# Optimization experiments

Hardware: AMD Instinct MI355X
Metric: run time of the kernel (lower is better)

The kernel has to match this reference:

```python
import jax, jax.numpy as jnp
import numpy as np

N = 100000   # nodes
E = 1600000  # edges
IN = 128     # in_feats
H = 3        # num_heads
D = 16       # out_feats per head
K = 3        # hops
NEG_SLOPE = 0.2
EPS = 1e-9


def leaky(x):
    return jnp.where(x >= 0, x, NEG_SLOPE * x)


def segment_softmax(e, idx, n):
    # e: [E, H] scores, softmax over edges sharing the same idx (node)
    m = jax.ops.segment_max(e, idx, num_segments=n)
    ex = jnp.exp(e - m[idx])
    s = jax.ops.segment_sum(ex, idx, num_segments=n)
    return ex / s[idx]


def feat_trans(h, i, norm_scales, offsets, pos_emb):
    # per-hop mean/var normalization (biased var) + position embedding
    mean = h.mean(axis=-1, keepdims=True)
    var = h.var(axis=-1, keepdims=True) + EPS
    h = (h - mean) * norm_scales[i] * jax.lax.rsqrt(var) + offsets[i]
    return h + pos_emb[:, :, i, :]


def setup_inputs() -> dict:
    key = jax.random.key(0)
    ks = jax.random.split(key, 10)
    s = 0.1
    feat = jax.random.normal(ks[0], (N, IN), jnp.float32)
    src = jax.random.randint(ks[1], (E,), 0, N)
    dst = jax.random.randint(ks[2], (E,), 0, N)
    fc_W = jax.random.normal(ks[3], (IN, H * D), jnp.float32) * s
    attn_l = jax.random.normal(ks[4], (1, H, D), jnp.float32) * s
    attn_r = jax.random.normal(ks[5], (1, H, D), jnp.float32) * s
    hop_attn_l = jax.random.normal(ks[6], (1, H, D), jnp.float32) * s
    hop_attn_r = jax.random.normal(ks[7], (1, H, D), jnp.float32) * s
    pos_emb = jax.random.normal(ks[8], (1, H, K + 1, D), jnp.float32) * s
    norm_scales = jnp.ones((K + 1, 1, H, D), jnp.float32)
    offsets = jnp.zeros((K + 1, 1, H, D), jnp.float32)
    bias = jnp.zeros((H * D,), jnp.float32)
    return dict(feat=feat, src=src, dst=dst, fc_W=fc_W, attn_l=attn_l,
                attn_r=attn_r, hop_attn_l=hop_attn_l, hop_attn_r=hop_attn_r,
                pos_emb=pos_emb, norm_scales=norm_scales, offsets=offsets,
                bias=bias)


def reference(feat, src, dst, fc_W, attn_l, attn_r, hop_attn_l, hop_attn_r,
              pos_emb, norm_scales, offsets, bias):
    ft = (feat @ fc_W).reshape(N, H, D)            # [N,H,D]
    el = (ft * attn_l).sum(-1)                      # [N,H]
    er = (ft * attn_r).sum(-1)                      # [N,H]
    e = leaky(el[src] + er[dst])                    # [E,H]
    a_dst = jnp.clip(segment_softmax(e, dst, N), EPS, None)
    a_src = jnp.clip(segment_softmax(e, src, N), EPS, None)
    a = jnp.sqrt(a_dst * a_src)                     # [E,H] symmetric attention

    h_query = feat_trans(ft, 0, norm_scales, offsets, pos_emb)[:, :, None, :]
    hstack = []
    cur = ft
    for k in range(1, K + 1):
        msg = cur[src] * a[:, :, None]              # [E,H,D]
        cur = jax.ops.segment_sum(msg, dst, num_segments=N)
        hstack.append(feat_trans(cur, k, norm_scales, offsets, pos_emb))
    hstack = jnp.stack(hstack, axis=2)              # [N,H,K,D]

    # hop attention (weight_style='HA')
    astack = (hstack * hop_attn_r[:, :, None, :]).sum(-1, keepdims=True) \
           + (h_query * hop_attn_l[:, :, None, :]).sum(-1, keepdims=True)
    astack = jax.nn.softmax(leaky(astack), axis=2)  # [N,H,K,1]
    rst = (hstack * astack).sum(axis=2)             # [N,H,D]
    return rst + bias.reshape(1, H, D)
```

## Files before the change

kernel.cpp:

```cpp
#include <hip/hip_runtime.h>
#include <hip/hip_bf16.h>

typedef __hip_bfloat16 bf16;

#define N_NODES 100000
#define N_EDGES 1600000
#define IN_F    128
#define HH      3
#define DD      16
#define HD      48
#define NEG_SLOPE 0.2f
#define EPS_V   1e-9f

#define NB      391
#define BW_SH   8
#define MS_T    8192

__device__ __forceinline__ float leaky(float x) { return x >= 0.f ? x : NEG_SLOPE * x; }
__device__ __forceinline__ float b2f(bf16 x) { return __bfloat162float(x); }

#define GR 32
__global__ __launch_bounds__(256) void k_gemm(const float* __restrict__ feat,
                                              const float* __restrict__ W,
                                              float* __restrict__ ft,
                                              bf16* __restrict__ ft16) {
    __shared__ float Ws[IN_F][HD];
    __shared__ float Fs[GR][IN_F + 1];
    int t = threadIdx.x;
    for (int i = t; i < IN_F * HD; i += 256) Ws[i / HD][i % HD] = W[i];
    int row0 = blockIdx.x * GR;
    for (int i = t; i < GR * IN_F; i += 256) {
        int r = i >> 7, c = i & 127;
        int gr = row0 + r;
        Fs[r][c] = (gr < N_NODES) ? feat[gr * IN_F + c] : 0.f;
    }
    __syncthreads();
    int r = t >> 3, cg = t & 7;
    float acc[6] = {0, 0, 0, 0, 0, 0};
    for (int k = 0; k < IN_F; ++k) {
        float a = Fs[r][k];
#pragma unroll
        for (int j = 0; j < 6; ++j) acc[j] += a * Ws[k][cg * 6 + j];
    }
    int gr = row0 + r;
    if (gr < N_NODES) {
#pragma unroll
        for (int j = 0; j < 6; ++j) {
            ft[gr * HD + cg * 6 + j] = acc[j];
            ft16[gr * HD + cg * 6 + j] = __float2bfloat16(acc[j]);
        }
    }
}

__global__ void k_eler(const float* __restrict__ ft, const float* __restrict__ attn_l,
                       const float* __restrict__ attn_r, float* __restrict__ el,
                       float* __restrict__ er) {
    int i = blockIdx.x * blockDim.x + threadIdx.x;
    if (i >= N_NODES * HH) return;
    int h = i % HH;
    float sl = 0.f, sr = 0.f;
#pragma unroll
    for (int d = 0; d < DD; ++d) {
        float v = ft[i * DD + d];
        sl += v * attn_l[h * DD + d];
        sr += v * attn_r[h * DD + d];
    }
    el[i] = sl;
    er[i] = sr;
}

__global__ __launch_bounds__(256) void k_bhist(const int* __restrict__ src,
                                               const int* __restrict__ dst,
                                               int* __restrict__ bcnt_s,
                                               int* __restrict__ bcnt_d) {
    __shared__ int ls[NB], ld_[NB];
    int t = threadIdx.x;
    for (int i = t; i < NB; i += 256) { ls[i] = 0; ld_[i] = 0; }
    __syncthreads();
    for (int e = blockIdx.x * 256 + t; e < N_EDGES; e += gridDim.x * 256) {
        atomicAdd(&ld_[dst[e] >> BW_SH], 1);
        atomicAdd(&ls[src[e] >> BW_SH], 1);
    }
    __syncthreads();
    for (int i = t; i < NB; i += 256) {
        if (ld_[i]) atomicAdd(&bcnt_d[i], ld_[i]);
        if (ls[i]) atomicAdd(&bcnt_s[i], ls[i]);
    }
}

__global__ __launch_bounds__(512) void k_bscan(const int* __restrict__ bcnt_d,
                                               int* __restrict__ bbase_d,
                                               const int* __restrict__ bcnt_s,
                                               int* __restrict__ bbase_s,
                                               int* __restrict__ rows_d,
                                               int* __restrict__ rows_s) {
    __shared__ int buf[512];
    const int* c = blockIdx.x ? bcnt_s : bcnt_d;
    int* o = blockIdx.x ? bbase_s : bbase_d;
    int t = threadIdx.x;
    int v = (t < NB) ? c[t] : 0;
    buf[t] = v;
    __syncthreads();
    for (int off = 1; off < 512; off <<= 1) {
        int u = (t >= off) ? buf[t - off] : 0;
        __syncthreads();
        buf[t] += u;
        __syncthreads();
    }
    if (t < NB) o[t] = buf[t] - v;
    if (t == NB - 1) o[NB] = buf[t];
    if (t == 0) {
        if (blockIdx.x) rows_s[N_NODES] = N_EDGES;
        else            rows_d[N_NODES] = N_EDGES;
    }
}

__global__ __launch_bounds__(256) void k_msplit(const int* __restrict__ src,
                                                const int* __restrict__ dst,
                                                const int* __restrict__ bbase_d,
                                                const int* __restrict__ bbase_s,
                                                int* __restrict__ bfill_d,
                                                int* __restrict__ bfill_s,
                                                unsigned* __restrict__ bkt_d,
                                                unsigned* __restrict__ bkt_s) {
    __shared__ int lcD[NB], lcS[NB], wbD[NB], wbS[NB], rkD[NB], rkS[NB];
    int t = threadIdx.x;
    int e0 = blockIdx.x * MS_T;
    int e1 = min(e0 + MS_T, N_EDGES);
    for (int i = t; i < NB; i += 256) { lcD[i] = 0; lcS[i] = 0; rkD[i] = 0; rkS[i] = 0; }
    __syncthreads();
    for (int e = e0 + t; e < e1; e += 256) {
        atomicAdd(&lcD[dst[e] >> BW_SH], 1);
        atomicAdd(&lcS[src[e] >> BW_SH], 1);
    }
    __syncthreads();
    for (int i = t; i < NB; i += 256) {
        wbD[i] = bbase_d[i] + (lcD[i] ? atomicAdd(&bfill_d[i], lcD[i]) : 0);
        wbS[i] = bbase_s[i] + (lcS[i] ? atomicAdd(&bfill_s[i], lcS[i]) : 0);
    }
    __syncthreads();
    for (int e = e0 + t; e < e1; e += 256) {
        int s = src[e], d = dst[e];
        int bd = d >> BW_SH, bs = s >> BW_SH;
        int rd = atomicAdd(&rkD[bd], 1);
        int rs = atomicAdd(&rkS[bs], 1);
        bkt_d[wbD[bd] + rd] = (unsigned)s | ((unsigned)(d & 255) << 17);
        bkt_s[wbS[bs] + rs] = (unsigned)d | ((unsigned)(s & 255) << 17);
    }
}

__global__ __launch_bounds__(256) void k_bfinal(const unsigned* __restrict__ bkt,
                                                const int* __restrict__ bbase,
                                                int* __restrict__ rows,
                                                int* __restrict__ outarr) {
    __shared__ int cnt[256], pre[256], rnk[256], wsum[4];
    int b = blockIdx.x, t = threadIdx.x;
    int base = bbase[b], end = bbase[b + 1];
    cnt[t] = 0; rnk[t] = 0;
    __syncthreads();
    for (int i = base + t; i < end; i += 256)
        atomicAdd(&cnt[(bkt[i] >> 17) & 255], 1);
    __syncthreads();
    int lane = t & 63, w = t >> 6;
    int v = cnt[t];
    int sc = v;
#pragma unroll
    for (int off = 1; off < 64; off <<= 1) {
        int u = __shfl_up(sc, off, 64);
        if (lane >= off) sc += u;
    }
    if (lane == 63) wsum[w] = sc;
    __syncthreads();
    int wpre = 0;
    for (int j = 0; j < w; ++j) wpre += wsum[j];
    int excl = wpre + sc - v;
    pre[t] = excl;
    int n = (b << BW_SH) + t;
    if (n < N_NODES) rows[n] = base + excl;
    __syncthreads();
    for (int i = base + t; i < end; i += 256) {
        unsigned u = bkt[i];
        int loc = (u >> 17) & 255;
        int r = atomicAdd(&rnk[loc], 1);
        outarr[base + pre[loc] + r] = (int)(u & 0x1FFFFu);
    }
}

__global__ __launch_bounds__(256) void k_seg_src(const int* __restrict__ dsts_s,
                                                 const int* __restrict__ rows_s,
                                                 const float* __restrict__ el,
                                                 const float* __restrict__ er,
                                                 float2* __restrict__ mssrc) {
    int wid = threadIdx.x >> 6, lane = threadIdx.x & 63;
    int n = blockIdx.x * 4 + wid;
    if (n >= N_NODES) return;
    int rs = rows_s[n], re = rows_s[n + 1];
    if (rs >= re) return;
    float el0 = el[n * 3 + 0], el1 = el[n * 3 + 1], el2 = el[n * 3 + 2];
    bool single = (re - rs) <= 64;
    float m0 = -INFINITY, m1 = -INFINITY, m2 = -INFINITY;
    float c0 = -INFINITY, c1 = -INFINITY, c2 = -INFINITY;
    for (int p0 = rs; p0 < re; p0 += 64) {
        int p = p0 + lane;
        bool act = p < re;
        int d = act ? dsts_s[p] : 0;
        float t0 = act ? leaky(el0 + er[d * 3 + 0]) : -INFINITY;
        float t1 = act ? leaky(el1 + er[d * 3 + 1]) : -INFINITY;
        float t2 = act ? leaky(el2 + er[d * 3 + 2]) : -INFINITY;
        if (single) { c0 = t0; c1 = t1; c2 = t2; }
        m0 = fmaxf(m0, t0); m1 = fmaxf(m1, t1); m2 = fmaxf(m2, t2);
    }
#pragma unroll
    for (int off = 1; off < 64; off <<= 1) {
        m0 = fmaxf(m0, __shfl_xor(m0, off));
        m1 = fmaxf(m1, __shfl_xor(m1, off));
        m2 = fmaxf(m2, __shfl_xor(m2, off));
    }
    float s0 = 0, s1 = 0, s2 = 0;
    if (single) {
        bool act = (rs + lane) < re;
        s0 = act ? expf(c0 - m0) : 0.f;
        s1 = act ? expf(c1 - m1) : 0.f;
        s2 = act ? expf(c2 - m2) : 0.f;
    } else {
        for (int p0 = rs; p0 < re; p0 += 64) {
            int p = p0 + lane;
            if (p < re) {
                int d = dsts_s[p];
                s0 += expf(leaky(el0 + er[d * 3 + 0]) - m0);
                s1 += expf(leaky(el1 + er[d * 3 + 1]) - m1);
                s2 += expf(leaky(el2 + er[d * 3 + 2]) - m2);
            }
        }
    }
#pragma unroll
    for (int off = 1; off < 64; off <<= 1) {
        s0 += __shfl_xor(s0, off);
        s1 += __shfl_xor(s1, off);
        s2 += __shfl_xor(s2, off);
    }
    if (lane == 0) {
        mssrc[n * 3 + 0] = make_float2(m0, s0);
        mssrc[n * 3 + 1] = make_float2(m1, s1);
        mssrc[n * 3 + 2] = make_float2(m2, s2);
    }
}

__global__ __launch_bounds__(256) void k_seg_dst_attn(const int* __restrict__ srcs_d,
                                                      const int* __restrict__ rows_d,
                                                      const float* __restrict__ el,
                                                      const float* __restrict__ er,
                                                      const float2* __restrict__ mssrc,
                                                      float* __restrict__ a_sorted) {
    int wid = threadIdx.x >> 6, lane = threadIdx.x & 63;
    int n = blockIdx.x * 4 + wid;
    if (n >= N_NODES) return;
    int rs = rows_d[n], re = rows_d[n + 1];
    if (rs >= re) return;
    float er0 = er[n * 3 + 0], er1 = er[n * 3 + 1], er2 = er[n * 3 + 2];
    bool single = (re - rs) <= 64;
    float m0 = -INFINITY, m1 = -INFINITY, m2 = -INFINITY;
    float c0 = -INFINITY, c1 = -INFINITY, c2 = -INFINITY;
    int scache = 0;
    for (int p0 = rs; p0 < re; p0 += 64) {
        int p = p0 + lane;
        bool act = p < re;
        int s = act ? srcs_d[p] : 0;
        if (single) scache = s;
        float t0 = act ? leaky(el[s * 3 + 0] + er0) : -INFINITY;
        float t1 = act ? leaky(el[s * 3 + 1] + er1) : -INFINITY;
        float t2 = act ? leaky(el[s * 3 + 2] + er2) : -INFINITY;
        if (single) { c0 = t0; c1 = t1; c2 = t2; }
        m0 = fmaxf(m0, t0); m1 = fmaxf(m1, t1); m2 = fmaxf(m2, t2);
    }
#pragma unroll
    for (int off = 1; off < 64; off <<= 1) {
        m0 = fmaxf(m0, __shfl_xor(m0, off));
        m1 = fmaxf(m1, __shfl_xor(m1, off));
        m2 = fmaxf(m2, __shfl_xor(m2, off));
    }
    float s0 = 0, s1 = 0, s2 = 0;
    if (single) {
        bool act = (rs + lane) < re;
        s0 = act ? expf(c0 - m0) : 0.f;
        s1 = act ? expf(c1 - m1) : 0.f;
        s2 = act ? expf(c2 - m2) : 0.f;
    } else {
        for (int p0 = rs; p0 < re; p0 += 64) {
            int p = p0 + lane;
            if (p < re) {
                int s = srcs_d[p];
                s0 += expf(leaky(el[s * 3 + 0] + er0) - m0);
                s1 += expf(leaky(el[s * 3 + 1] + er1) - m1);
                s2 += expf(leaky(el[s * 3 + 2] + er2) - m2);
            }
        }
    }
#pragma unroll
    for (int off = 1; off < 64; off <<= 1) {
        s0 += __shfl_xor(s0, off);
        s1 += __shfl_xor(s1, off);
        s2 += __shfl_xor(s2, off);
    }
    float i0 = 1.f / s0, i1 = 1.f / s1, i2 = 1.f / s2;
    for (int p0 = rs; p0 < re; p0 += 64) {
        int p = p0 + lane;
        if (p >= re) break;
        int s = single ? scache : srcs_d[p];
        float t0, t1, t2;
        if (single) { t0 = c0; t1 = c1; t2 = c2; }
        else {
            t0 = leaky(el[s * 3 + 0] + er0);
            t1 = leaky(el[s * 3 + 1] + er1);
            t2 = leaky(el[s * 3 + 2] + er2);
        }
        float2 a0 = mssrc[s * 3 + 0], a1 = mssrc[s * 3 + 1], a2 = mssrc[s * 3 + 2];
        float d0 = fmaxf(expf(t0 - m0) * i0, EPS_V);
        float d1 = fmaxf(expf(t1 - m1) * i1, EPS_V);
        float d2 = fmaxf(expf(t2 - m2) * i2, EPS_V);
        float u0 = fmaxf(expf(t0 - a0.x) / a0.y, EPS_V);
        float u1 = fmaxf(expf(t1 - a1.x) / a1.y, EPS_V);
        float u2 = fmaxf(expf(t2 - a2.x) / a2.y, EPS_V);
        a_sorted[p * 3 + 0] = sqrtf(d0 * u0);
        a_sorted[p * 3 + 1] = sqrtf(d1 * u1);
        a_sorted[p * 3 + 2] = sqrtf(d2 * u2);
    }
}

__global__ __launch_bounds__(256) void k_hop(const bf16* __restrict__ cur,
                                             const float* __restrict__ a_sorted,
                                             const int* __restrict__ rowstart,
                                             const int* __restrict__ src_sorted,
                                             bf16* __restrict__ out) {
    int wid = threadIdx.x >> 6, lane = threadIdx.x & 63;
    int n = blockIdx.x * 4 + wid;
    if (n >= N_NODES) return;
    if (lane >= HD) return;
    int h = lane >> 4;
    int rs = rowstart[n], re = rowstart[n + 1];
    float acc = 0.f;
    int p = rs;
    for (; p + 8 <= re; p += 8) {
        int s[8];
#pragma unroll
        for (int j = 0; j < 8; ++j) s[j] = src_sorted[p + j];
        float a[8];
#pragma unroll
        for (int j = 0; j < 8; ++j) a[j] = a_sorted[(p + j) * HH + h];
        float v[8];
#pragma unroll
        for (int j = 0; j < 8; ++j) v[j] = b2f(cur[s[j] * HD + lane]);
#pragma unroll
        for (int j = 0; j < 8; ++j) acc += a[j] * v[j];
    }
    if (p < re) {
        int cnt = re - p;
        int s[8];
#pragma unroll
        for (int j = 0; j < 8; ++j) s[j] = (j < cnt) ? src_sorted[p + j] : 0;
        float a[8];
#pragma unroll
        for (int j = 0; j < 8; ++j) a[j] = (j < cnt) ? a_sorted[(p + j) * HH + h] : 0.f;
        float v[8];
#pragma unroll
        for (int j = 0; j < 8; ++j) v[j] = (j < cnt) ? b2f(cur[s[j] * HD + lane]) : 0.f;
#pragma unroll
        for (int j = 0; j < 8; ++j) acc += a[j] * v[j];
    }
    out[n * HD + lane] = __float2bfloat16(acc);
}

__global__ void k_final(const float* __restrict__ ft, const bf16* __restrict__ cur1,
                        const bf16* __restrict__ cur2, const bf16* __restrict__ cur3,
                        const float* __restrict__ hop_l, const float* __restrict__ hop_r,
                        const float* __restrict__ pos_emb, const float* __restrict__ scales,
                        const float* __restrict__ offs, const float* __restrict__ bias,
                        float* __restrict__ out) {
    int i = blockIdx.x * blockDim.x + threadIdx.x;
    if (i >= N_NODES * HH) return;
    int h = i % HH;
    float hk[4][DD];
#pragma unroll
    for (int k = 0; k < 4; ++k) {
        float x[DD];
#pragma unroll
        for (int d = 0; d < DD; ++d) {
            x[d] = (k == 0) ? ft[(size_t)i * DD + d]
                 : (k == 1) ? b2f(cur1[(size_t)i * DD + d])
                 : (k == 2) ? b2f(cur2[(size_t)i * DD + d])
                            : b2f(cur3[(size_t)i * DD + d]);
        }
        float m = 0.f;
#pragma unroll
        for (int d = 0; d < DD; ++d) m += x[d];
        m *= (1.f / DD);
        float v2 = 0.f;
#pragma unroll
        for (int d = 0; d < DD; ++d) {
            float c = x[d] - m;
            v2 += c * c;
        }
        v2 = v2 * (1.f / DD) + EPS_V;
        float rsq = rsqrtf(v2);
#pragma unroll
        for (int d = 0; d < DD; ++d) {
            hk[k][d] = (x[d] - m) * scales[k * HD + h * DD + d] * rsq +
                       offs[k * HD + h * DD + d] + pos_emb[h * 64 + k * DD + d];
        }
    }
    float al = 0.f;
#pragma unroll
    for (int d = 0; d < DD; ++d) al += hk[0][d] * hop_l[h * DD + d];
    float ar[3], mx = -1e30f;
#pragma unroll
    for (int k = 0; k < 3; ++k) {
        float s = 0.f;
#pragma unroll
        for (int d = 0; d < DD; ++d) s += hk[k + 1][d] * hop_r[h * DD + d];
        ar[k] = leaky(s + al);
        mx = fmaxf(mx, ar[k]);
    }
    float den = 0.f, wgt[3];
#pragma unroll
    for (int k = 0; k < 3; ++k) {
        wgt[k] = expf(ar[k] - mx);
        den += wgt[k];
    }
#pragma unroll
    for (int k = 0; k < 3; ++k) wgt[k] /= den;
#pragma unroll
    for (int d = 0; d < DD; ++d) {
        float o = hk[1][d] * wgt[0] + hk[2][d] * wgt[1] + hk[3][d] * wgt[2] +
                  bias[h * DD + d];
        out[i * DD + d] = o;
    }
}

#define OFF_FT     0u
#define OFF_FT16   4800000u
#define OFF_EL     7200000u
#define OFF_ER     7500000u
#define OFF_MSSRC  7800000u
#define OFF_BCNT   8400000u
#define OFF_BBASE  8401600u
#define OFF_ROWD   8402400u
#define OFF_ROWS_  8502402u
#define OFF_BKTD   8602404u
#define OFF_BKTS   10202404u
#define OFF_SRCSD  11802404u
#define OFF_DSTSS  13402404u
#define OFF_ASORT  15002404u
#define OFF_CUR1   19802404u
#define OFF_CUR2   22202404u
#define OFF_CUR3   24602404u
#define WS_FLOATS  27002404u

extern "C" void kernel_launch(void* const* d_in, const int* in_sizes, int n_in,
                              void* d_out, int out_size, void* d_ws, size_t ws_size,
                              hipStream_t stream) {
    if (ws_size < (size_t)WS_FLOATS * 4) return;

    const float* feat   = (const float*)d_in[0];
    const int*   src    = (const int*)d_in[1];
    const int*   dst    = (const int*)d_in[2];
    const float* fc_W   = (const float*)d_in[3];
    const float* attn_l = (const float*)d_in[4];
    const float* attn_r = (const float*)d_in[5];
    const float* hop_l  = (const float*)d_in[6];
    const float* hop_r  = (const float*)d_in[7];
    const float* pos    = (const float*)d_in[8];
    const float* scal   = (const float*)d_in[9];
    const float* offs   = (const float*)d_in[10];
    const float* bias   = (const float*)d_in[11];
    float* out = (float*)d_out;

    float* ws = (float*)d_ws;
    float*    ft      = ws + OFF_FT;
    bf16*     ft16    = (bf16*)(ws + OFF_FT16);
    float*    el      = ws + OFF_EL;
    float*    er      = ws + OFF_ER;
    float2*   mssrc   = (float2*)(ws + OFF_MSSRC);
    int*      bcnt_d  = (int*)(ws + OFF_BCNT);
    int*      bcnt_s  = bcnt_d + 400;
    int*      bfill_d = bcnt_d + 800;
    int*      bfill_s = bcnt_d + 1200;
    int*      bbase_d = (int*)(ws + OFF_BBASE);
    int*      bbase_s = bbase_d + 400;
    int*      rows_d  = (int*)(ws + OFF_ROWD);
    int*      rows_s  = (int*)(ws + OFF_ROWS_);
    unsigned* bkt_d   = (unsigned*)(ws + OFF_BKTD);
    unsigned* bkt_s   = (unsigned*)(ws + OFF_BKTS);
    int*      srcs_d  = (int*)(ws + OFF_SRCSD);
    int*      dsts_s  = (int*)(ws + OFF_DSTSS);
    float*    a_sorted= ws + OFF_ASORT;
    bf16*     cur1    = (bf16*)(ws + OFF_CUR1);
    bf16*     cur2    = (bf16*)(ws + OFF_CUR2);
    bf16*     cur3    = (bf16*)(ws + OFF_CUR3);

    hipMemsetAsync(ws + OFF_BCNT, 0, 1600 * 4, stream);

    k_gemm<<<(N_NODES + GR - 1) / GR, 256, 0, stream>>>(feat, fc_W, ft, ft16);
    k_eler<<<(N_NODES * HH + 255) / 256, 256, 0, stream>>>(ft, attn_l, attn_r, el, er);

    k_bhist<<<64, 256, 0, stream>>>(src, dst, bcnt_s, bcnt_d);
    k_bscan<<<2, 512, 0, stream>>>(bcnt_d, bbase_d, bcnt_s, bbase_s, rows_d, rows_s);
    k_msplit<<<(N_EDGES + MS_T - 1) / MS_T, 256, 0, stream>>>(src, dst, bbase_d, bbase_s,
                                                              bfill_d, bfill_s, bkt_d, bkt_s);
    k_bfinal<<<NB, 256, 0, stream>>>(bkt_d, bbase_d, rows_d, srcs_d);
    k_bfinal<<<NB, 256, 0, stream>>>(bkt_s, bbase_s, rows_s, dsts_s);

    k_seg_src<<<(N_NODES + 3) / 4, 256, 0, stream>>>(dsts_s, rows_s, el, er, mssrc);
    k_seg_dst_attn<<<(N_NODES + 3) / 4, 256, 0, stream>>>(srcs_d, rows_d, el, er,
                                                          mssrc, a_sorted);
    k_hop<<<(N_NODES + 3) / 4, 256, 0, stream>>>(ft16, a_sorted, rows_d, srcs_d, cur1);
    k_hop<<<(N_NODES + 3) / 4, 256, 0, stream>>>(cur1, a_sorted, rows_d, srcs_d, cur2);
    k_hop<<<(N_NODES + 3) / 4, 256, 0, stream>>>(cur2, a_sorted, rows_d, srcs_d, cur3);
    k_final<<<(N_NODES * HH + 255) / 256, 256, 0, stream>>>(ft, cur1, cur2, cur3, hop_l,
                                                            hop_r, pos, scal, offs, bias,
                                                            out);
}
```

Before: 543.8 us.

## Rewrite projection GEMM as one-row-per-thread and vectorize edge histogram with more blocks

The feature projection kernel drops its shared-memory tiles and has each thread compute one full 48-wide output row. It loads the row with float4 and reads weights through uniform global loads, meant to hit cache or scalar loads. The bucket histogram now reads src/dst as int4 and launches 400 blocks instead of 64, to raise memory parallelism. The new GEMM keeps 48 accumulators per thread, which raises register pressure. Its per-thread row stride gives uncoalesced feat loads, and its bf16 stores are scattered.

```diff
diff --git a/kernel.cpp b/kernel.cpp
--- a/kernel.cpp
+++ b/kernel.cpp
@@ -19,37 +19,35 @@
 __device__ __forceinline__ float leaky(float x) { return x >= 0.f ? x : NEG_SLOPE * x; }
 __device__ __forceinline__ float b2f(bf16 x) { return __bfloat162float(x); }
 
-#define GR 32
 __global__ __launch_bounds__(256) void k_gemm(const float* __restrict__ feat,
                                               const float* __restrict__ W,
                                               float* __restrict__ ft,
                                               bf16* __restrict__ ft16) {
-    __shared__ float Ws[IN_F][HD];
-    __shared__ float Fs[GR][IN_F + 1];
-    int t = threadIdx.x;
-    for (int i = t; i < IN_F * HD; i += 256) Ws[i / HD][i % HD] = W[i];
-    int row0 = blockIdx.x * GR;
-    for (int i = t; i < GR * IN_F; i += 256) {
-        int r = i >> 7, c = i & 127;
-        int gr = row0 + r;
-        Fs[r][c] = (gr < N_NODES) ? feat[gr * IN_F + c] : 0.f;
-    }
-    __syncthreads();
-    int r = t >> 3, cg = t & 7;
-    float acc[6] = {0, 0, 0, 0, 0, 0};
-    for (int k = 0; k < IN_F; ++k) {
-        float a = Fs[r][k];
-#pragma unroll
-        for (int j = 0; j < 6; ++j) acc[j] += a * Ws[k][cg * 6 + j];
-    }
-    int gr = row0 + r;
-    if (gr < N_NODES) {
-#pragma unroll
-        for (int j = 0; j < 6; ++j) {
-            ft[gr * HD + cg * 6 + j] = acc[j];
-            ft16[gr * HD + cg * 6 + j] = __float2bfloat16(acc[j]);
-        }
-    }
+    int row = blockIdx.x * 256 + threadIdx.x;
+    if (row >= N_NODES) return;
+    float acc[HD];
+#pragma unroll
+    for (int c = 0; c < HD; ++c) acc[c] = 0.f;
+    const float4* frow = (const float4*)(feat + (size_t)row * IN_F);
+    for (int k4 = 0; k4 < IN_F / 4; ++k4) {
+        float4 f = frow[k4];
+        int k = k4 * 4;
+#pragma unroll
+        for (int c = 0; c < HD; ++c) acc[c] += f.x * W[(k + 0) * HD + c];
+#pragma unroll
+        for (int c = 0; c < HD; ++c) acc[c] += f.y * W[(k + 1) * HD + c];
+#pragma unroll
+        for (int c = 0; c < HD; ++c) acc[c] += f.z * W[(k + 2) * HD + c];
+#pragma unroll
+        for (int c = 0; c < HD; ++c) acc[c] += f.w * W[(k + 3) * HD + c];
+    }
+    float4* orow = (float4*)(ft + (size_t)row * HD);
+#pragma unroll
+    for (int c = 0; c < HD / 4; ++c)
+        orow[c] = make_float4(acc[4 * c], acc[4 * c + 1], acc[4 * c + 2], acc[4 * c + 3]);
+    bf16* o16 = ft16 + (size_t)row * HD;
+#pragma unroll
+    for (int c = 0; c < HD; ++c) o16[c] = __float2bfloat16(acc[c]);
 }
 
 __global__ void k_eler(const float* __restrict__ ft, const float* __restrict__ attn_l,
@@ -69,17 +67,26 @@
     er[i] = sr;
 }
 
-__global__ __launch_bounds__(256) void k_bhist(const int* __restrict__ src,
-                                               const int* __restrict__ dst,
+__global__ __launch_bounds__(256) void k_bhist(const int4* __restrict__ src4,
+                                               const int4* __restrict__ dst4,
                                                int* __restrict__ bcnt_s,
                                                int* __restrict__ bcnt_d) {
     __shared__ int ls[NB], ld_[NB];
     int t = threadIdx.x;
     for (int i = t; i < NB; i += 256) { ls[i] = 0; ld_[i] = 0; }
     __syncthreads();
-    for (int e = blockIdx.x * 256 + t; e < N_EDGES; e += gridDim.x * 256) {
-        atomicAdd(&ld_[dst[e] >> BW_SH], 1);
-        atomicAdd(&ls[src[e] >> BW_SH], 1);
+    const int NE4 = N_EDGES / 4;
+    for (int e = blockIdx.x * 256 + t; e < NE4; e += gridDim.x * 256) {
+        int4 d = dst4[e];
+        atomicAdd(&ld_[d.x >> BW_SH], 1);
+        atomicAdd(&ld_[d.y >> BW_SH], 1);
+        atomicAdd(&ld_[d.z >> BW_SH], 1);
+        atomicAdd(&ld_[d.w >> BW_SH], 1);
+        int4 s = src4[e];
+        atomicAdd(&ls[s.x >> BW_SH], 1);
+        atomicAdd(&ls[s.y >> BW_SH], 1);
+        atomicAdd(&ls[s.z >> BW_SH], 1);
+        atomicAdd(&ls[s.w >> BW_SH], 1);
     }
     __syncthreads();
     for (int i = t; i < NB; i += 256) {
@@ -499,10 +506,10 @@
 
     hipMemsetAsync(ws + OFF_BCNT, 0, 1600 * 4, stream);
 
-    k_gemm<<<(N_NODES + GR - 1) / GR, 256, 0, stream>>>(feat, fc_W, ft, ft16);
+    k_gemm<<<(N_NODES + 255) / 256, 256, 0, stream>>>(feat, fc_W, ft, ft16);
     k_eler<<<(N_NODES * HH + 255) / 256, 256, 0, stream>>>(ft, attn_l, attn_r, el, er);
 
-    k_bhist<<<64, 256, 0, stream>>>(src, dst, bcnt_s, bcnt_d);
+    k_bhist<<<400, 256, 0, stream>>>((const int4*)src, (const int4*)dst, bcnt_s, bcnt_d);
     k_bscan<<<2, 512, 0, stream>>>(bcnt_d, bbase_d, bcnt_s, bbase_s, rows_d, rows_s);
     k_msplit<<<(N_EDGES + MS_T - 1) / MS_T, 256, 0, stream>>>(src, dst, bbase_d, bbase_s,
                                                               bfill_d, bfill_s, bkt_d, bkt_s);
```

After: 493.6 us. 1.1x faster.
